# Optimization experiments

Hardware: AMD Instinct MI355X
Metric: run time of the kernel (lower is better)

## Reference

```python
import jax, jax.numpy as jnp
import numpy as np

N, T, C, D, H, O = 1024, 12, 32, 64, 256, 64


def setup_inputs() -> dict:
    key = jax.random.key(0)
    ks = jax.random.split(key, 8)
    s = lambda fan: 1.0 / np.sqrt(fan)
    return {
        "x": jax.random.normal(ks[0], (N, T, C, D), jnp.float32),
        # dense per-timestep semantic adjacency [T,1,N,N]; rand -> strictly positive weights
        "semantic_data": jax.random.uniform(ks[1], (T, 1, N, N), dtype=jnp.float32),
        # node_mlp: Linear(D,H) -> ReLU -> Linear(H,O) -> ReLU ; node_out_net: Linear(O,O)
        "W1": jax.random.uniform(ks[2], (D, H), jnp.float32, -s(D), s(D)),
        "b1": jax.random.uniform(ks[3], (H,), jnp.float32, -s(D), s(D)),
        "W2": jax.random.uniform(ks[4], (H, O), jnp.float32, -s(H), s(H)),
        "b2": jax.random.uniform(ks[5], (O,), jnp.float32, -s(H), s(H)),
        "Wo": jax.random.uniform(ks[6], (O, O), jnp.float32, -s(O), s(O)),
        "bo": jax.random.uniform(ks[7], (O,), jnp.float32, -s(O), s(O)),
    }


def reference(x, semantic_data, W1, b1, W2, b2, Wo, bo):
    # dense_to_sparse(A[t]) yields edges (r, j) with weight A[t, r, j].
    # NodeModel computes (note: BOTH gather and scatter use col=j):
    #   geo_sum[j]   = sum_r A[t,r,j] * x[j]  = colsum[t,j] * x[j]
    #   geo_denom[j] = sum_r A[t,r,j]         = colsum[t,j]
    # Zero entries of A contribute nothing, so dense column-sums are exact.
    A = semantic_data[:, 0]                    # [T, N, N]
    colsum = A.sum(axis=1)                     # sum over rows r -> [T, N]
    denom = colsum.T[:, :, None, None]         # [N, T, 1, 1] aligned with x [N,T,C,D]
    mask = denom != 0
    safe = jnp.where(mask, denom, 1.0)
    # geo_agg = x + geo_sum/geo_denom; NaN (0/0 where no incoming edges) -> 0
    geo_agg = jnp.where(mask, x + (denom * x) / safe, 0.0)
    h = jax.nn.relu(geo_agg @ W1 + b1)         # [N, T, C, H]
    h = jax.nn.relu(h @ W2 + b2)               # [N, T, C, O]
    return h @ Wo + bo                         # [N, T, C, O]
```

## Files before the change

### kernel.cpp

```cpp
#include <hip/hip_runtime.h>
#include <hip/hip_bf16.h>
#include <stdint.h>


using short8 = __attribute__((ext_vector_type(8))) short;
using f32x4  = __attribute__((ext_vector_type(4))) float;

#define NN 1024
#define TT 12
#define CC 32
#define DD 64
#define HH 256
#define OO 64
#define MTOT (NN * TT * CC)

__device__ __forceinline__ short f2bf(float f) {
    union { __hip_bfloat16 h; short s; } u;
    u.h = __float2bfloat16(f);
    return u.s;
}

__global__ void prepack_kernel(const float* __restrict__ W1, const float* __restrict__ W2,
                               const float* __restrict__ Wo, unsigned short* __restrict__ wf) {
    int fidx = blockIdx.x;
    int l = threadIdx.x;
    int r = l & 15, g = l >> 4;
    unsigned short vals[8];
    if (fidx < 32) {
        int hblk = fidx >> 1, ks = fidx & 1;
        #pragma unroll
        for (int j = 0; j < 8; ++j) {
            int d = ks * 32 + g * 8 + j, h = hblk * 16 + r;
            vals[j] = (unsigned short)f2bf(W1[d * HH + h]);
        }
    } else if (fidx < 64) {
        int f = fidx - 32, nt2 = f >> 3, ksg = f & 7;
        #pragma unroll
        for (int j = 0; j < 8; ++j) {
            int h = ksg * 32 + g * 8 + j, o = nt2 * 16 + r;
            vals[j] = (unsigned short)f2bf(W2[h * OO + o]);
        }
    } else {
        int f = fidx - 64, nt3 = f >> 1, ks3 = f & 1;
        #pragma unroll
        for (int j = 0; j < 8; ++j) {
            int o1 = ks3 * 32 + g * 8 + j, o2 = nt3 * 16 + r;
            vals[j] = (unsigned short)f2bf(Wo[o1 * OO + o2]);
        }
    }
    unsigned short* dst = wf + (size_t)fidx * 512 + l * 8;
    #pragma unroll
    for (int j = 0; j < 8; ++j) dst[j] = vals[j];
}

__launch_bounds__(256, 4)
__global__ void fused_mlp_kernel(const float* __restrict__ x,
                                 const unsigned short* __restrict__ wf,
                                 const float* __restrict__ b1, const float* __restrict__ b2,
                                 const float* __restrict__ bo, float* __restrict__ out) {
    __shared__ short sBuf[4][32 * 128];
    const int tid = threadIdx.x;
    const int w = tid >> 6, l = tid & 63;
    const int r = l & 15, g = l >> 4;
    const int m0 = (blockIdx.x * 4 + w) * 32;

    short8 a1[2][2];
    #pragma unroll
    for (int ms = 0; ms < 2; ++ms) {
        #pragma unroll
        for (int ks = 0; ks < 2; ++ks) {
            const float* px = x + (size_t)(m0 + ms * 16 + r) * DD + ks * 32 + g * 8;
            float4 u0 = *(const float4*)px;
            float4 u1 = *(const float4*)(px + 4);
            float vv[8] = {u0.x, u0.y, u0.z, u0.w, u1.x, u1.y, u1.z, u1.w};
            short8 a;
            #pragma unroll
            for (int j = 0; j < 8; ++j) a[j] = f2bf(2.0f * vv[j]);
            a1[ms][ks] = a;
        }
    }

    const short8* wf8 = (const short8*)wf;
    short* myH = sBuf[w];
    f32x4 acc2[2][4] = {};

    #pragma unroll
    for (int half = 0; half < 2; ++half) {
        #pragma unroll
        for (int nt = 0; nt < 8; ++nt) {
            int hblk = half * 8 + nt;
            f32x4 acc0 = {0.f, 0.f, 0.f, 0.f}, accA = {0.f, 0.f, 0.f, 0.f};
            #pragma unroll
            for (int ks = 0; ks < 2; ++ks) {
                short8 bfr = wf8[(hblk * 2 + ks) * 64 + l];
                acc0 = __builtin_amdgcn_mfma_f32_16x16x32_bf16(a1[0][ks], bfr, acc0, 0, 0, 0);
                accA = __builtin_amdgcn_mfma_f32_16x16x32_bf16(a1[1][ks], bfr, accA, 0, 0, 0);
            }
            float bias = b1[hblk * 16 + r];
            #pragma unroll
            for (int ms = 0; ms < 2; ++ms) {
                f32x4 acc = ms ? accA : acc0;
                #pragma unroll
                for (int reg = 0; reg < 4; ++reg) {
                    float v = acc[reg] + bias;
                    v = v > 0.f ? v : 0.f;
                    int m = ms * 16 + 4 * g + reg;
                    int xh5 = ((2 * (g & 1) + (reg >> 1)) & 3) << 5;
                    int addr = m * 256 + ((2 * r) ^ ((reg & 1) << 4)) + ((nt << 5) ^ xh5);
                    myH[addr >> 1] = f2bf(v);
                }
            }
        }
        asm volatile("s_waitcnt lgkmcnt(0)" ::: "memory");
        short8 a2[2][4];
        #pragma unroll
        for (int ms = 0; ms < 2; ++ms) {
            #pragma unroll
            for (int k2 = 0; k2 < 4; ++k2) {
                int row = ms * 16 + r;
                int addr = row * 256 + ((g ^ (r & 3)) << 4) + ((k2 ^ ((r >> 2) & 1)) << 6);
                a2[ms][k2] = *reinterpret_cast<const short8*>(myH + (addr >> 1));
            }
        }
        #pragma unroll
        for (int nt2 = 0; nt2 < 4; ++nt2) {
            #pragma unroll
            for (int k2 = 0; k2 < 4; ++k2) {
                short8 bfr = wf8[(32 + nt2 * 8 + half * 4 + k2) * 64 + l];
                acc2[0][nt2] = __builtin_amdgcn_mfma_f32_16x16x32_bf16(a2[0][k2], bfr, acc2[0][nt2], 0, 0, 0);
                acc2[1][nt2] = __builtin_amdgcn_mfma_f32_16x16x32_bf16(a2[1][k2], bfr, acc2[1][nt2], 0, 0, 0);
            }
        }
    }

    #pragma unroll
    for (int nt2 = 0; nt2 < 4; ++nt2) {
        float bias = b2[nt2 * 16 + r];
        #pragma unroll
        for (int ms = 0; ms < 2; ++ms) {
            #pragma unroll
            for (int reg = 0; reg < 4; ++reg) {
                float v = acc2[ms][nt2][reg] + bias;
                v = v > 0.f ? v : 0.f;
                int m = ms * 16 + 4 * g + reg;
                int xh5 = ((2 * (g & 1) + (reg >> 1)) & 3) << 5;
                int addr = m * 128 + ((2 * r) ^ ((reg & 1) << 4)) + ((nt2 << 5) ^ xh5);
                myH[addr >> 1] = f2bf(v);
            }
        }
    }
    asm volatile("s_waitcnt lgkmcnt(0)" ::: "memory");
    short8 a3[2][2];
    #pragma unroll
    for (int ms = 0; ms < 2; ++ms) {
        #pragma unroll
        for (int k3 = 0; k3 < 2; ++k3) {
            int row = ms * 16 + r;
            int addr = row * 128 + ((g ^ (r & 3)) << 4) + ((k3 ^ ((r >> 2) & 1)) << 6);
            a3[ms][k3] = *reinterpret_cast<const short8*>(myH + (addr >> 1));
        }
    }
    #pragma unroll
    for (int nt3 = 0; nt3 < 4; ++nt3) {
        f32x4 c0 = {0.f, 0.f, 0.f, 0.f}, c1 = {0.f, 0.f, 0.f, 0.f};
        #pragma unroll
        for (int k3 = 0; k3 < 2; ++k3) {
            short8 bfr = wf8[(64 + nt3 * 2 + k3) * 64 + l];
            c0 = __builtin_amdgcn_mfma_f32_16x16x32_bf16(a3[0][k3], bfr, c0, 0, 0, 0);
            c1 = __builtin_amdgcn_mfma_f32_16x16x32_bf16(a3[1][k3], bfr, c1, 0, 0, 0);
        }
        float bias = bo[nt3 * 16 + r];
        #pragma unroll
        for (int reg = 0; reg < 4; ++reg) {
            out[(size_t)(m0 + 4 * g + reg) * OO + nt3 * 16 + r] = c0[reg] + bias;
            out[(size_t)(m0 + 16 + 4 * g + reg) * OO + nt3 * 16 + r] = c1[reg] + bias;
        }
    }
}

extern "C" void kernel_launch(void* const* d_in, const int* in_sizes, int n_in,
                              void* d_out, int out_size, void* d_ws, size_t ws_size,
                              hipStream_t stream) {
    const float* x   = (const float*)d_in[0];
    const float* W1  = (const float*)d_in[2];
    const float* b1  = (const float*)d_in[3];
    const float* W2  = (const float*)d_in[4];
    const float* b2  = (const float*)d_in[5];
    const float* Wo  = (const float*)d_in[6];
    const float* bo  = (const float*)d_in[7];
    float* out = (float*)d_out;

    unsigned short* wf = (unsigned short*)d_ws;

    prepack_kernel<<<dim3(72), dim3(64), 0, stream>>>(W1, W2, Wo, wf);
    fused_mlp_kernel<<<dim3(MTOT / 128), dim3(256), 0, stream>>>(x, wf, b1, b2, bo, out);
}
```

Baseline: 277.6 us.

## Split hidden layer into quarters to halve LDS and raise occupancy

```diff
diff --git a/kernel.cpp b/kernel.cpp
--- a/kernel.cpp
+++ b/kernel.cpp
@@ -53,12 +53,12 @@
     for (int j = 0; j < 8; ++j) dst[j] = vals[j];
 }
 
-__launch_bounds__(256, 4)
+__launch_bounds__(256, 6)
 __global__ void fused_mlp_kernel(const float* __restrict__ x,
                                  const unsigned short* __restrict__ wf,
                                  const float* __restrict__ b1, const float* __restrict__ b2,
                                  const float* __restrict__ bo, float* __restrict__ out) {
-    __shared__ short sBuf[4][32 * 128];
+    __shared__ short sBuf[4][32 * 64];
     const int tid = threadIdx.x;
     const int w = tid >> 6, l = tid & 63;
     const int r = l & 15, g = l >> 4;
@@ -85,10 +85,10 @@
     f32x4 acc2[2][4] = {};
 
     #pragma unroll
-    for (int half = 0; half < 2; ++half) {
-        #pragma unroll
-        for (int nt = 0; nt < 8; ++nt) {
-            int hblk = half * 8 + nt;
+    for (int q = 0; q < 4; ++q) {
+        #pragma unroll
+        for (int nt = 0; nt < 4; ++nt) {
+            int hblk = q * 4 + nt;
             f32x4 acc0 = {0.f, 0.f, 0.f, 0.f}, accA = {0.f, 0.f, 0.f, 0.f};
             #pragma unroll
             for (int ks = 0; ks < 2; ++ks) {
@@ -105,30 +105,29 @@
                     float v = acc[reg] + bias;
                     v = v > 0.f ? v : 0.f;
                     int m = ms * 16 + 4 * g + reg;
-                    int xh5 = ((2 * (g & 1) + (reg >> 1)) & 3) << 5;
-                    int addr = m * 256 + ((2 * r) ^ ((reg & 1) << 4)) + ((nt << 5) ^ xh5);
+                    int addr = m * 128 + ((nt * 32 + 2 * r) ^ ((m & 7) << 4));
                     myH[addr >> 1] = f2bf(v);
                 }
             }
         }
         asm volatile("s_waitcnt lgkmcnt(0)" ::: "memory");
-        short8 a2[2][4];
+        short8 a2[2][2];
         #pragma unroll
         for (int ms = 0; ms < 2; ++ms) {
             #pragma unroll
-            for (int k2 = 0; k2 < 4; ++k2) {
+            for (int kq = 0; kq < 2; ++kq) {
                 int row = ms * 16 + r;
-                int addr = row * 256 + ((g ^ (r & 3)) << 4) + ((k2 ^ ((r >> 2) & 1)) << 6);
-                a2[ms][k2] = *reinterpret_cast<const short8*>(myH + (addr >> 1));
+                int addr = row * 128 + ((kq * 64 + g * 16) ^ ((row & 7) << 4));
+                a2[ms][kq] = *reinterpret_cast<const short8*>(myH + (addr >> 1));
             }
         }
         #pragma unroll
         for (int nt2 = 0; nt2 < 4; ++nt2) {
             #pragma unroll
-            for (int k2 = 0; k2 < 4; ++k2) {
-                short8 bfr = wf8[(32 + nt2 * 8 + half * 4 + k2) * 64 + l];
-                acc2[0][nt2] = __builtin_amdgcn_mfma_f32_16x16x32_bf16(a2[0][k2], bfr, acc2[0][nt2], 0, 0, 0);
-                acc2[1][nt2] = __builtin_amdgcn_mfma_f32_16x16x32_bf16(a2[1][k2], bfr, acc2[1][nt2], 0, 0, 0);
+            for (int kq = 0; kq < 2; ++kq) {
+                short8 bfr = wf8[(32 + nt2 * 8 + q * 2 + kq) * 64 + l];
+                acc2[0][nt2] = __builtin_amdgcn_mfma_f32_16x16x32_bf16(a2[0][kq], bfr, acc2[0][nt2], 0, 0, 0);
+                acc2[1][nt2] = __builtin_amdgcn_mfma_f32_16x16x32_bf16(a2[1][kq], bfr, acc2[1][nt2], 0, 0, 0);
             }
         }
     }
@@ -143,8 +142,7 @@
                 float v = acc2[ms][nt2][reg] + bias;
                 v = v > 0.f ? v : 0.f;
                 int m = ms * 16 + 4 * g + reg;
-                int xh5 = ((2 * (g & 1) + (reg >> 1)) & 3) << 5;
-                int addr = m * 128 + ((2 * r) ^ ((reg & 1) << 4)) + ((nt2 << 5) ^ xh5);
+                int addr = m * 128 + ((nt2 * 32 + 2 * r) ^ ((m & 7) << 4));
                 myH[addr >> 1] = f2bf(v);
             }
         }
@@ -156,10 +154,11 @@
         #pragma unroll
         for (int k3 = 0; k3 < 2; ++k3) {
             int row = ms * 16 + r;
-            int addr = row * 128 + ((g ^ (r & 3)) << 4) + ((k3 ^ ((r >> 2) & 1)) << 6);
+            int addr = row * 128 + ((k3 * 64 + g * 16) ^ ((row & 7) << 4));
             a3[ms][k3] = *reinterpret_cast<const short8*>(myH + (addr >> 1));
         }
     }
+    f32x4 cc[2][4];
     #pragma unroll
     for (int nt3 = 0; nt3 < 4; ++nt3) {
         f32x4 c0 = {0.f, 0.f, 0.f, 0.f}, c1 = {0.f, 0.f, 0.f, 0.f};
@@ -171,9 +170,16 @@
         }
         float bias = bo[nt3 * 16 + r];
         #pragma unroll
+        for (int reg = 0; reg < 4; ++reg) { cc[0][nt3][reg] = c0[reg] + bias; cc[1][nt3][reg] = c1[reg] + bias; }
+    }
+    #pragma unroll
+    for (int ms = 0; ms < 2; ++ms) {
+        #pragma unroll
         for (int reg = 0; reg < 4; ++reg) {
-            out[(size_t)(m0 + 4 * g + reg) * OO + nt3 * 16 + r] = c0[reg] + bias;
-            out[(size_t)(m0 + 16 + 4 * g + reg) * OO + nt3 * 16 + r] = c1[reg] + bias;
+            size_t rowbase = (size_t)(m0 + ms * 16 + 4 * g + reg) * OO;
+            #pragma unroll
+            for (int nt3 = 0; nt3 < 4; ++nt3)
+                out[rowbase + nt3 * 16 + r] = cc[ms][nt3][reg];
         }
     }
 }
```

Result: slower. 356.9 us (+28.6%).
